# Kernel optimization log

Hardware: AMD Instinct MI355X
Metric: run time of the kernel (lower is better)

Reference implementation:

```python
import jax, jax.numpy as jnp
import numpy as np

N = 320      # num_seq == num_res (pair representation)
C = 128      # num_channels
H = 4        # num_head
D = 32       # qkv_dim = max(C // H, 16)
EPS = 1e-5   # torch LayerNorm default eps
MASK_FILL = -1e9


def setup_inputs() -> dict:
    key = jax.random.key(0)
    ks = jax.random.split(key, 9)
    s = 0.02
    return {
        "act": jax.random.normal(ks[0], (N, N, C), jnp.float32),
        "pair_mask": jax.random.randint(ks[1], (N, N), 0, 2).astype(jnp.int32),
        "ln_gamma": jnp.ones((C,), jnp.float32),
        "ln_beta": jnp.zeros((C,), jnp.float32),
        "w_pair_bias": jax.random.normal(ks[2], (C, H), jnp.float32) * s,  # Linear(C->H, no bias)
        "wq": jax.random.normal(ks[3], (C, H, D), jnp.float32) * s,
        "wk": jax.random.normal(ks[4], (C, H, D), jnp.float32) * s,
        "wv": jax.random.normal(ks[5], (C, H, D), jnp.float32) * s,
        "w_gate": jax.random.normal(ks[6], (C, C), jnp.float32) * s,  # used as act @ W (matches torch.matmul(act, weight))
        "w_out": jax.random.normal(ks[7], (C, C), jnp.float32) * s,   # nn.Linear weight [out,in]; applied as x @ W.T
    }


def reference(act, pair_mask, ln_gamma, ln_beta, w_pair_bias, wq, wk, wv, w_gate, w_out):
    # LayerNorm over channels
    mu = jnp.mean(act, axis=-1, keepdims=True)
    var = jnp.var(act, axis=-1, keepdims=True)
    x = (act - mu) * jax.lax.rsqrt(var + EPS) * ln_gamma + ln_beta  # [N, N, C]

    # Pair-derived nonbatched bias: Linear(C->H) then permute(2,0,1) -> [H, N, N]
    bias = jnp.einsum('qkc,ch->hqk', x, w_pair_bias)

    # pair_mask.permute(1,0)[:, None, None, :] -> [N, 1, 1, N] bool
    mask = (pair_mask.T > 0)[:, None, None, :]

    # QKV projections via einsum '...i,ijk->...jk'
    scale = wq.shape[-1] ** -0.5
    q = jnp.einsum('bqc,chd->bqhd', x, wq) * scale  # [N, N, H, D]
    k = jnp.einsum('bkc,chd->bkhd', x, wk)
    v = jnp.einsum('bkc,chd->bkhd', x, wv)

    logits = jnp.einsum('bqhd,bkhd->bhqk', q, k) + bias[None]  # [N, H, N, N]
    logits = jnp.where(mask, logits, MASK_FILL)
    weights = jax.nn.softmax(logits, axis=-1)
    wa = jnp.einsum('bhqk,bkhd->bqhd', weights, v)  # [N, N, H, D]
    wa = wa.reshape(wa.shape[0], wa.shape[1], -1)   # [N, N, C]

    gate = jax.nn.sigmoid(x @ w_gate)               # torch.matmul(act, gating_query.weight)
    out = (wa * gate) @ w_out.T                     # output_projection (Linear, no bias)
    return out
```

## Files before the change

kernel.cpp:

```cpp
#include <hip/hip_runtime.h>
#include <cstdio>
#include <cstdint>


#define NSEQ 320
#define CCH  128
#define NN   102400
#define QK_SCALE 0.17677669529663687f
#define LN_EPS 1e-5f
#define NEG_BIG -1e9f

typedef __bf16 bf16x8 __attribute__((ext_vector_type(8)));
typedef float  f32x4  __attribute__((ext_vector_type(4)));

__device__ __forceinline__ unsigned short f2bf(float f) {
    unsigned int u = __float_as_uint(f);
    unsigned int r = (u + 0x7FFFu + ((u >> 16) & 1u)) >> 16;
    return (unsigned short)r;
}
__device__ __forceinline__ float bf2f(unsigned short h) {
    return __uint_as_float(((unsigned int)h) << 16);
}

__global__ __launch_bounds__(256) void prep_kernel(
    const float* __restrict__ wq, const float* __restrict__ wk, const float* __restrict__ wv,
    const float* __restrict__ wg, const float* __restrict__ wpb, const float* __restrict__ wo,
    const int* __restrict__ pmask,
    unsigned short* __restrict__ wcat, unsigned short* __restrict__ woutb, int* __restrict__ maskT)
{
    int idx = blockIdx.x * 256 + threadIdx.x;
    if (idx < 576 * 128) {
        int n = idx >> 7, c = idx & 127;
        float v;
        if      (n < 128) v = wq[c * 128 + n] * QK_SCALE;
        else if (n < 256) v = wk[c * 128 + (n - 128)];
        else if (n < 384) v = wv[c * 128 + (n - 256)];
        else if (n < 512) v = wg[c * 128 + (n - 384)];
        else if (n < 516) v = wpb[c * 4 + (n - 512)];
        else              v = 0.f;
        wcat[idx] = f2bf(v);
    } else if (idx < 576 * 128 + 128 * 128) {
        int i = idx - 576 * 128;
        woutb[i] = f2bf(wo[i]);
    } else if (idx < 576 * 128 + 128 * 128 + NN) {
        int i = idx - (576 * 128 + 128 * 128);
        int b = i / NSEQ, k = i - b * NSEQ;
        maskT[i] = pmask[k * NSEQ + b];
    }
}

__global__ __launch_bounds__(256, 4) void ln_proj_kernel(
    const float* __restrict__ act, const float* __restrict__ gamma, const float* __restrict__ beta,
    const unsigned short* __restrict__ wcat,
    unsigned short* __restrict__ qh, unsigned short* __restrict__ kh, unsigned short* __restrict__ vT,
    unsigned short* __restrict__ gh, float* __restrict__ biasS)
{
    __shared__ __align__(16) float          fs[64 * 132];
    __shared__ __align__(16) unsigned short A_lds[64 * 136];
    unsigned short* B_lds = (unsigned short*)fs;

    const int tid  = threadIdx.x;
    const int row0 = blockIdx.x * 64;
    const int bidx = row0 / NSEQ;
    const int qoff = row0 % NSEQ;

    const float4* actv = (const float4*)(act + (size_t)row0 * 128);
    #pragma unroll
    for (int it = 0; it < 8; ++it) {
        int f = it * 256 + tid;
        int row = f >> 5, c4 = f & 31;
        float4 v = actv[f];
        *(float4*)&fs[row * 132 + c4 * 4] = v;
    }
    __syncthreads();

    {
        int row = tid >> 2, seg = tid & 3;
        const float* rp = &fs[row * 132 + seg * 32];
        float vals[32];
        float s = 0.f, sq = 0.f;
        #pragma unroll
        for (int i = 0; i < 32; ++i) { float v = rp[i]; vals[i] = v; s += v; sq += v * v; }
        s  += __shfl_xor(s, 1);  sq += __shfl_xor(sq, 1);
        s  += __shfl_xor(s, 2);  sq += __shfl_xor(sq, 2);
        float mean = s * (1.f / 128.f);
        float var  = sq * (1.f / 128.f) - mean * mean;
        float rstd = rsqrtf(var + LN_EPS);
        #pragma unroll
        for (int j = 0; j < 4; ++j) {
            int c0 = seg * 32 + j * 8;
            float4 g0 = *(const float4*)&gamma[c0];
            float4 g1 = *(const float4*)&gamma[c0 + 4];
            float4 b0 = *(const float4*)&beta[c0];
            float4 b1 = *(const float4*)&beta[c0 + 4];
            union { uint4 u; unsigned short us[8]; } pk;
            pk.us[0] = f2bf((vals[j*8+0] - mean) * rstd * g0.x + b0.x);
            pk.us[1] = f2bf((vals[j*8+1] - mean) * rstd * g0.y + b0.y);
            pk.us[2] = f2bf((vals[j*8+2] - mean) * rstd * g0.z + b0.z);
            pk.us[3] = f2bf((vals[j*8+3] - mean) * rstd * g0.w + b0.w);
            pk.us[4] = f2bf((vals[j*8+4] - mean) * rstd * g1.x + b1.x);
            pk.us[5] = f2bf((vals[j*8+5] - mean) * rstd * g1.y + b1.y);
            pk.us[6] = f2bf((vals[j*8+6] - mean) * rstd * g1.z + b1.z);
            pk.us[7] = f2bf((vals[j*8+7] - mean) * rstd * g1.w + b1.w);
            *(uint4*)&A_lds[row * 136 + c0] = pk.u;
        }
    }
    __syncthreads();

    const int wave = tid >> 6, lane = tid & 63, l15 = lane & 15, l4 = lane >> 4;
    bf16x8 afrag[4];
    #pragma unroll
    for (int kc = 0; kc < 4; ++kc)
        afrag[kc] = *(const bf16x8*)&A_lds[(wave * 16 + l15) * 136 + kc * 32 + l4 * 8];

    for (int nt = 0; nt < 9; ++nt) {
        #pragma unroll
        for (int it = 0; it < 4; ++it) {
            int f = it * 256 + tid;
            int row = f >> 4, c16 = f & 15;
            uint4 u = *(const uint4*)&wcat[(nt * 64 + row) * 128 + c16 * 8];
            *(uint4*)&B_lds[row * 136 + c16 * 8] = u;
        }
        __syncthreads();

        f32x4 acc[4];
        #pragma unroll
        for (int ns = 0; ns < 4; ++ns) { f32x4 z = {0.f,0.f,0.f,0.f}; acc[ns] = z; }
        #pragma unroll
        for (int ns = 0; ns < 4; ++ns)
            #pragma unroll
            for (int kc = 0; kc < 4; ++kc) {
                bf16x8 bfrag = *(const bf16x8*)&B_lds[(ns * 16 + l15) * 136 + kc * 32 + l4 * 8];
                acc[ns] = __builtin_amdgcn_mfma_f32_16x16x32_bf16(afrag[kc], bfrag, acc[ns], 0, 0, 0);
            }

        if (nt == 4 || nt == 5) {
            int key0 = qoff + wave * 16 + l4 * 4;
            #pragma unroll
            for (int ns = 0; ns < 4; ++ns) {
                int j  = nt * 64 + ns * 16 + l15 - 256;
                int hh = j >> 5, d = j & 31;
                ushort4 pk;
                pk.x = f2bf(acc[ns][0]); pk.y = f2bf(acc[ns][1]);
                pk.z = f2bf(acc[ns][2]); pk.w = f2bf(acc[ns][3]);
                *(ushort4*)&vT[((size_t)(bidx * 4 + hh) * 32 + d) * NSEQ + key0] = pk;
            }
            __syncthreads();
        } else if (nt == 8) {
            #pragma unroll
            for (int ns = 0; ns < 4; ++ns) {
                int j = nt * 64 + ns * 16 + l15;
                if (j < 516) {
                    #pragma unroll
                    for (int reg = 0; reg < 4; ++reg) {
                        int r  = row0 + wave * 16 + l4 * 4 + reg;
                        int hh = j - 512;
                        int q  = r / NSEQ, key = r - q * NSEQ;
                        int qm = q & 15,  kl  = key & 15;
                        size_t a = (((size_t)(hh * 20 + (q >> 4)) * 20 + (key >> 4)) << 8)
                                 + ((qm >> 2) << 6) + (kl << 2) + (qm & 3);
                        biasS[a] = acc[ns][reg];
                    }
                }
            }
        } else {
            float* scratch = (float*)A_lds;
            #pragma unroll
            for (int ns = 0; ns < 4; ++ns)
                #pragma unroll
                for (int reg = 0; reg < 4; ++reg)
                    scratch[(wave * 16 + l4 * 4 + reg) * 68 + ns * 16 + l15] = acc[ns][reg];
            __syncthreads();

            int rrow = tid >> 2, c16 = tid & 3;
            int q = qoff + rrow;
            float f[16];
            #pragma unroll
            for (int i = 0; i < 4; ++i)
                *(float4*)&f[i * 4] = *(const float4*)&scratch[rrow * 68 + c16 * 16 + i * 4];

            int jbase = nt * 64 + c16 * 16;
            int cls   = jbase >> 7;
            int jl    = jbase & 127;
            int hh = jl >> 5, d0 = jl & 31;
            unsigned short* dst = (cls == 0) ? qh : (cls == 1) ? kh : gh;
            if (cls == 3) {
                #pragma unroll
                for (int i = 0; i < 16; ++i) f[i] = 1.f / (1.f + __expf(-f[i]));
            }
            union { uint4 u[2]; unsigned short us[16]; } pk;
            #pragma unroll
            for (int i = 0; i < 16; ++i) pk.us[i] = f2bf(f[i]);
            size_t base = ((size_t)(bidx * 4 + hh) * NSEQ + q) * 32 + d0;
            *(uint4*)&dst[base]     = pk.u[0];
            *(uint4*)&dst[base + 8] = pk.u[1];
        }
    }
}

__global__ __launch_bounds__(256, 4) void attn_kernel(
    const unsigned short* __restrict__ qh, const unsigned short* __restrict__ kh,
    const unsigned short* __restrict__ vT, const unsigned short* __restrict__ gh,
    const float* __restrict__ biasS, const int* __restrict__ maskT,
    unsigned short* __restrict__ waG)
{
    __shared__ __align__(16) unsigned short Klds[320 * 36];
    __shared__ __align__(16) unsigned short Pb[4][2][16 * 36];

    const int tid  = threadIdx.x;
    const int bid  = blockIdx.x;
    const int xcd  = bid & 7;
    const int loc  = bid >> 3;
    const int qblk = loc % 5;
    const int g    = (loc / 5) * 8 + xcd;
    const int b    = g >> 2;
    const int h    = g & 3;
    const int wave = tid >> 6, lane = tid & 63, l15 = lane & 15, l4 = lane >> 4;

    const size_t hb  = (size_t)g * NSEQ;
    const size_t hbv = (size_t)g * 32;

    {
        const uint4* src = (const uint4*)(kh + hb * 32);
        #pragma unroll
        for (int it = 0; it < 5; ++it) {
            int idx = it * 256 + tid;
            int key = idx >> 2, part = idx & 3;
            uint4 u = src[idx];
            *(uint4*)&Klds[key * 36 + part * 8] = u;
        }
    }

    const int qrow = qblk * 64 + wave * 16;
    const int qb16 = qblk * 4 + wave;

    bf16x8 aQ = *(const bf16x8*)&qh[(hb + qrow + l15) * 32 + l4 * 8];
    const float* bsw = biasS + (size_t)(h * 20 + qb16) * 20 * 256 + lane * 4;
    const int*   mp  = maskT + b * NSEQ + l15;

    f32x4 s[20];
    #pragma unroll
    for (int t = 0; t < 20; ++t) s[t] = *(const f32x4*)&bsw[t * 256];

    __syncthreads();

    #pragma unroll
    for (int t = 0; t < 20; ++t) {
        bf16x8 bK = *(const bf16x8*)&Klds[(t * 16 + l15) * 36 + l4 * 8];
        s[t] = __builtin_amdgcn_mfma_f32_16x16x32_bf16(aQ, bK, s[t], 0, 0, 0);
    }

    #pragma unroll
    for (int t = 0; t < 20; ++t) {
        int m = mp[t * 16];
        #pragma unroll
        for (int r = 0; r < 4; ++r) s[t][r] = m ? s[t][r] : NEG_BIG;
    }

    #pragma unroll
    for (int r = 0; r < 4; ++r) {
        float mx = -3.4e38f;
        #pragma unroll
        for (int t = 0; t < 20; ++t) mx = fmaxf(mx, s[t][r]);
        mx = fmaxf(mx, __shfl_xor(mx, 1));
        mx = fmaxf(mx, __shfl_xor(mx, 2));
        mx = fmaxf(mx, __shfl_xor(mx, 4));
        mx = fmaxf(mx, __shfl_xor(mx, 8));
        float l = 0.f;
        #pragma unroll
        for (int t = 0; t < 20; ++t) { float p = __expf(s[t][r] - mx); s[t][r] = p; l += p; }
        l += __shfl_xor(l, 1); l += __shfl_xor(l, 2); l += __shfl_xor(l, 4); l += __shfl_xor(l, 8);
        float wv = 1.f / l;
        #pragma unroll
        for (int t = 0; t < 20; ++t) s[t][r] *= wv;
    }

    unsigned short* pb[2] = { Pb[wave][0], Pb[wave][1] };
    #pragma unroll
    for (int tt = 0; tt < 2; ++tt)
        #pragma unroll
        for (int r = 0; r < 4; ++r)
            pb[0][(l4 * 4 + r) * 36 + tt * 16 + l15] = f2bf(s[tt][r]);

    f32x4 acc[2];
    { f32x4 z = {0.f,0.f,0.f,0.f}; acc[0] = z; acc[1] = z; }
    #pragma unroll
    for (int kc = 0; kc < 10; ++kc) {
        bf16x8 aW = *(const bf16x8*)&pb[kc & 1][l15 * 36 + l4 * 8];
        if (kc < 9) {
            unsigned short* nxt = pb[(kc + 1) & 1];
            #pragma unroll
            for (int tt = 0; tt < 2; ++tt)
                #pragma unroll
                for (int r = 0; r < 4; ++r)
                    nxt[(l4 * 4 + r) * 36 + tt * 16 + l15] = f2bf(s[2 * kc + 2 + tt][r]);
        }
        #pragma unroll
        for (int ns = 0; ns < 2; ++ns) {
            bf16x8 bV = *(const bf16x8*)&vT[(hbv + ns * 16 + l15) * NSEQ + kc * 32 + l4 * 8];
            acc[ns] = __builtin_amdgcn_mfma_f32_16x16x32_bf16(aW, bV, acc[ns], 0, 0, 0);
        }
    }

    #pragma unroll
    for (int ns = 0; ns < 2; ++ns)
        #pragma unroll
        for (int r = 0; r < 4; ++r) {
            int q   = qrow + l4 * 4 + r;
            int col = ns * 16 + l15;
            float gv = bf2f(gh[(hb + q) * 32 + col]);
            waG[(hb + q) * 32 + col] = f2bf(acc[ns][r] * gv);
        }
}

__global__ __launch_bounds__(256, 4) void out_proj_kernel(
    const unsigned short* __restrict__ waG, const unsigned short* __restrict__ woutb,
    float* __restrict__ out)
{
    __shared__ __align__(16) unsigned short A_lds[64 * 136];
    __shared__ __align__(16) unsigned short B_lds[128 * 136];
    const int tid  = threadIdx.x;
    const int row0 = blockIdx.x * 64;
    const int bidx = row0 / NSEQ;
    const int qoff = row0 % NSEQ;

    #pragma unroll
    for (int it = 0; it < 4; ++it) {
        int f = it * 256 + tid;
        int row = f >> 4, c16 = f & 15;
        int hh = c16 >> 2, d0 = (c16 & 3) * 8;
        uint4 u = *(const uint4*)&waG[((size_t)(bidx * 4 + hh) * NSEQ + (qoff + row)) * 32 + d0];
        *(uint4*)&A_lds[row * 136 + c16 * 8] = u;
    }
    #pragma unroll
    for (int it = 0; it < 8; ++it) {
        int f = it * 256 + tid;
        int row = f >> 4, c16 = f & 15;
        uint4 u = *(const uint4*)&woutb[f * 8];
        *(uint4*)&B_lds[row * 136 + c16 * 8] = u;
    }
    __syncthreads();

    const int wave = tid >> 6, lane = tid & 63, l15 = lane & 15, l4 = lane >> 4;
    bf16x8 afrag[4];
    #pragma unroll
    for (int kc = 0; kc < 4; ++kc)
        afrag[kc] = *(const bf16x8*)&A_lds[(wave * 16 + l15) * 136 + kc * 32 + l4 * 8];
    f32x4 acc[8];
    #pragma unroll
    for (int ns = 0; ns < 8; ++ns) { f32x4 z = {0.f,0.f,0.f,0.f}; acc[ns] = z; }
    #pragma unroll
    for (int ns = 0; ns < 8; ++ns)
        #pragma unroll
        for (int kc = 0; kc < 4; ++kc) {
            bf16x8 bfrag = *(const bf16x8*)&B_lds[(ns * 16 + l15) * 136 + kc * 32 + l4 * 8];
            acc[ns] = __builtin_amdgcn_mfma_f32_16x16x32_bf16(afrag[kc], bfrag, acc[ns], 0, 0, 0);
        }
    #pragma unroll
    for (int ns = 0; ns < 8; ++ns)
        #pragma unroll
        for (int reg = 0; reg < 4; ++reg) {
            int r = row0 + wave * 16 + l4 * 4 + reg;
            out[(size_t)r * 128 + ns * 16 + l15] = acc[ns][reg];
        }
}

extern "C" void kernel_launch(void* const* d_in, const int* in_sizes, int n_in,
                              void* d_out, int out_size, void* d_ws, size_t ws_size,
                              hipStream_t stream)
{
    (void)in_sizes; (void)n_in; (void)out_size;
    const float* act  = (const float*)d_in[0];
    const int*   pmsk = (const int*)d_in[1];
    const float* gam  = (const float*)d_in[2];
    const float* bet  = (const float*)d_in[3];
    const float* wpb  = (const float*)d_in[4];
    const float* wq   = (const float*)d_in[5];
    const float* wk   = (const float*)d_in[6];
    const float* wv   = (const float*)d_in[7];
    const float* wg   = (const float*)d_in[8];
    const float* wo   = (const float*)d_in[9];
    float* out = (float*)d_out;

    char* ws = (char*)d_ws;
    unsigned short* wcat  = (unsigned short*)(ws + 0);
    unsigned short* woutb = (unsigned short*)(ws + 147456);
    int*            maskT = (int*)           (ws + 180224);
    float*          biasS = (float*)         (ws + 589824);
    unsigned short* qh    = (unsigned short*)(ws + 2228224);
    unsigned short* kh    = (unsigned short*)(ws + 28442624);
    unsigned short* vT    = (unsigned short*)(ws + 54657024);
    unsigned short* gh    = (unsigned short*)(ws + 80871424);
    unsigned short* waG   = (unsigned short*)(ws + 107085824);
    if (ws_size < 133300224ull) {
        fprintf(stderr, "kernel_launch: ws too small (%zu < 133300224)\n", ws_size);
        return;
    }

    prep_kernel    <<<752,  256, 0, stream>>>(wq, wk, wv, wg, wpb, wo, pmsk, wcat, woutb, maskT);
    ln_proj_kernel <<<1600, 256, 0, stream>>>(act, gam, bet, wcat, qh, kh, vT, gh, biasS);
    attn_kernel    <<<6400, 256, 0, stream>>>(qh, kh, vT, gh, biasS, maskT, waG);
    out_proj_kernel<<<1600, 256, 0, stream>>>(waG, woutb, out);
}
```

Measured before the change: 265.6 us.

## Restructure projection, attention softmax and prep kernels with larger tiles and online softmax

The projection kernel now handles 128 rows per block, reading act directly from global memory instead of staging it in LDS, so each weight tile loaded into LDS is reused for two row tiles. The attention kernel switches to a transposed MFMA orientation (K times Q, V times P) and processes keys in two chunks with an online softmax, which lowers register pressure and allows an occupancy hint of 5. The mask transpose in the prep kernel now goes through an LDS tile so both its reads and writes are coalesced. LDS row strides change from 136/36 to 138/34/38 to reduce bank conflicts. The changes to the biasS layout and the write orientation have to stay consistent between the kernels, which adds correctness risk.

Result: slower. 370.1 us (+39.4%).

```diff
diff --git a/kernel.cpp b/kernel.cpp
--- a/kernel.cpp
+++ b/kernel.cpp
@@ -28,59 +28,68 @@
     const int* __restrict__ pmask,
     unsigned short* __restrict__ wcat, unsigned short* __restrict__ woutb, int* __restrict__ maskT)
 {
-    int idx = blockIdx.x * 256 + threadIdx.x;
-    if (idx < 576 * 128) {
-        int n = idx >> 7, c = idx & 127;
-        float v;
-        if      (n < 128) v = wq[c * 128 + n] * QK_SCALE;
-        else if (n < 256) v = wk[c * 128 + (n - 128)];
-        else if (n < 384) v = wv[c * 128 + (n - 256)];
-        else if (n < 512) v = wg[c * 128 + (n - 384)];
-        else if (n < 516) v = wpb[c * 4 + (n - 512)];
-        else              v = 0.f;
-        wcat[idx] = f2bf(v);
-    } else if (idx < 576 * 128 + 128 * 128) {
-        int i = idx - 576 * 128;
-        woutb[i] = f2bf(wo[i]);
-    } else if (idx < 576 * 128 + 128 * 128 + NN) {
-        int i = idx - (576 * 128 + 128 * 128);
-        int b = i / NSEQ, k = i - b * NSEQ;
-        maskT[i] = pmask[k * NSEQ + b];
-    }
-}
-
-__global__ __launch_bounds__(256, 4) void ln_proj_kernel(
+    const int tid = threadIdx.x;
+    if (blockIdx.x < 352) {
+        int idx = blockIdx.x * 256 + tid;
+        if (idx < 576 * 128) {
+            int n = idx >> 7, c = idx & 127;
+            float v;
+            if      (n < 128) v = wq[c * 128 + n] * QK_SCALE;
+            else if (n < 256) v = wk[c * 128 + (n - 128)];
+            else if (n < 384) v = wv[c * 128 + (n - 256)];
+            else if (n < 512) v = wg[c * 128 + (n - 384)];
+            else if (n < 516) v = wpb[c * 4 + (n - 512)];
+            else              v = 0.f;
+            wcat[idx] = f2bf(v);
+        } else {
+            int i = idx - 576 * 128;
+            woutb[i] = f2bf(wo[i]);
+        }
+    } else {
+        __shared__ int tile[64][65];
+        int tb = blockIdx.x - 352;
+        int ti = tb / 5, tj = tb % 5;
+        #pragma unroll
+        for (int it = 0; it < 16; ++it) {
+            int e = it * 256 + tid;
+            int r = e >> 6, c = e & 63;
+            tile[r][c] = pmask[(ti * 64 + r) * NSEQ + tj * 64 + c];
+        }
+        __syncthreads();
+        #pragma unroll
+        for (int it = 0; it < 16; ++it) {
+            int e = it * 256 + tid;
+            int r = e >> 6, c = e & 63;
+            maskT[(tj * 64 + r) * NSEQ + ti * 64 + c] = tile[c][r];
+        }
+    }
+}
+
+__global__ __launch_bounds__(256, 3) void ln_proj_kernel(
     const float* __restrict__ act, const float* __restrict__ gamma, const float* __restrict__ beta,
     const unsigned short* __restrict__ wcat,
     unsigned short* __restrict__ qh, unsigned short* __restrict__ kh, unsigned short* __restrict__ vT,
     unsigned short* __restrict__ gh, float* __restrict__ biasS)
 {
-    __shared__ __align__(16) float          fs[64 * 132];
-    __shared__ __align__(16) unsigned short A_lds[64 * 136];
-    unsigned short* B_lds = (unsigned short*)fs;
+    __shared__ __align__(16) unsigned short A_lds[128 * 138];
+    __shared__ __align__(16) unsigned short B_lds[64 * 138];
 
     const int tid  = threadIdx.x;
-    const int row0 = blockIdx.x * 64;
-    const int bidx = row0 / NSEQ;
-    const int qoff = row0 % NSEQ;
-
-    const float4* actv = (const float4*)(act + (size_t)row0 * 128);
-    #pragma unroll
-    for (int it = 0; it < 8; ++it) {
-        int f = it * 256 + tid;
-        int row = f >> 5, c4 = f & 31;
-        float4 v = actv[f];
-        *(float4*)&fs[row * 132 + c4 * 4] = v;
-    }
-    __syncthreads();
-
-    {
-        int row = tid >> 2, seg = tid & 3;
-        const float* rp = &fs[row * 132 + seg * 32];
+    const int row0 = blockIdx.x * 128;
+    const int wave = tid >> 6, lane = tid & 63, l15 = lane & 15, l4 = lane >> 4;
+
+    #pragma unroll
+    for (int p = 0; p < 2; ++p) {
+        int row = p * 64 + (tid >> 2), seg = tid & 3;
+        const float* rp = act + (size_t)(row0 + row) * 128 + seg * 32;
         float vals[32];
         float s = 0.f, sq = 0.f;
         #pragma unroll
-        for (int i = 0; i < 32; ++i) { float v = rp[i]; vals[i] = v; s += v; sq += v * v; }
+        for (int i = 0; i < 8; ++i) {
+            float4 v = *(const float4*)&rp[i * 4];
+            vals[i*4+0]=v.x; vals[i*4+1]=v.y; vals[i*4+2]=v.z; vals[i*4+3]=v.w;
+            s += v.x+v.y+v.z+v.w; sq += v.x*v.x+v.y*v.y+v.z*v.z+v.w*v.w;
+        }
         s  += __shfl_xor(s, 1);  sq += __shfl_xor(sq, 1);
         s  += __shfl_xor(s, 2);  sq += __shfl_xor(sq, 2);
         float mean = s * (1.f / 128.f);
@@ -102,16 +111,19 @@
             pk.us[5] = f2bf((vals[j*8+5] - mean) * rstd * g1.y + b1.y);
             pk.us[6] = f2bf((vals[j*8+6] - mean) * rstd * g1.z + b1.z);
             pk.us[7] = f2bf((vals[j*8+7] - mean) * rstd * g1.w + b1.w);
-            *(uint4*)&A_lds[row * 136 + c0] = pk.u;
+            *(uint4*)&A_lds[row * 138 + c0] = pk.u;
         }
     }
     __syncthreads();
 
-    const int wave = tid >> 6, lane = tid & 63, l15 = lane & 15, l4 = lane >> 4;
-    bf16x8 afrag[4];
-    #pragma unroll
-    for (int kc = 0; kc < 4; ++kc)
-        afrag[kc] = *(const bf16x8*)&A_lds[(wave * 16 + l15) * 136 + kc * 32 + l4 * 8];
+    bf16x8 afrag[2][4];
+    #pragma unroll
+    for (int tl = 0; tl < 2; ++tl)
+        #pragma unroll
+        for (int kc = 0; kc < 4; ++kc)
+            afrag[tl][kc] = *(const bf16x8*)&A_lds[(tl * 64 + wave * 16 + l15) * 138 + kc * 32 + l4 * 8];
+
+    float* scratch = (float*)A_lds;
 
     for (int nt = 0; nt < 9; ++nt) {
         #pragma unroll
@@ -119,93 +131,99 @@
             int f = it * 256 + tid;
             int row = f >> 4, c16 = f & 15;
             uint4 u = *(const uint4*)&wcat[(nt * 64 + row) * 128 + c16 * 8];
-            *(uint4*)&B_lds[row * 136 + c16 * 8] = u;
+            *(uint4*)&B_lds[row * 138 + c16 * 8] = u;
         }
         __syncthreads();
 
-        f32x4 acc[4];
-        #pragma unroll
-        for (int ns = 0; ns < 4; ++ns) { f32x4 z = {0.f,0.f,0.f,0.f}; acc[ns] = z; }
+        f32x4 acc[2][4];
+        #pragma unroll
+        for (int tl = 0; tl < 2; ++tl)
+            #pragma unroll
+            for (int ns = 0; ns < 4; ++ns) { f32x4 z = {0.f,0.f,0.f,0.f}; acc[tl][ns] = z; }
         #pragma unroll
         for (int ns = 0; ns < 4; ++ns)
             #pragma unroll
             for (int kc = 0; kc < 4; ++kc) {
-                bf16x8 bfrag = *(const bf16x8*)&B_lds[(ns * 16 + l15) * 136 + kc * 32 + l4 * 8];
-                acc[ns] = __builtin_amdgcn_mfma_f32_16x16x32_bf16(afrag[kc], bfrag, acc[ns], 0, 0, 0);
+                bf16x8 bfrag = *(const bf16x8*)&B_lds[(ns * 16 + l15) * 138 + kc * 32 + l4 * 8];
+                #pragma unroll
+                for (int tl = 0; tl < 2; ++tl)
+                    acc[tl][ns] = __builtin_amdgcn_mfma_f32_16x16x32_bf16(afrag[tl][kc], bfrag, acc[tl][ns], 0, 0, 0);
             }
 
         if (nt == 4 || nt == 5) {
-            int key0 = qoff + wave * 16 + l4 * 4;
-            #pragma unroll
-            for (int ns = 0; ns < 4; ++ns) {
-                int j  = nt * 64 + ns * 16 + l15 - 256;
-                int hh = j >> 5, d = j & 31;
-                ushort4 pk;
-                pk.x = f2bf(acc[ns][0]); pk.y = f2bf(acc[ns][1]);
-                pk.z = f2bf(acc[ns][2]); pk.w = f2bf(acc[ns][3]);
-                *(ushort4*)&vT[((size_t)(bidx * 4 + hh) * 32 + d) * NSEQ + key0] = pk;
+            #pragma unroll
+            for (int tl = 0; tl < 2; ++tl) {
+                int R = row0 + tl * 64 + wave * 16 + l4 * 4;
+                int bb = R / NSEQ, key0 = R - bb * NSEQ;
+                #pragma unroll
+                for (int ns = 0; ns < 4; ++ns) {
+                    int j  = nt * 64 + ns * 16 + l15 - 256;
+                    int hh = j >> 5, d = j & 31;
+                    ushort4 pk;
+                    pk.x = f2bf(acc[tl][ns][0]); pk.y = f2bf(acc[tl][ns][1]);
+                    pk.z = f2bf(acc[tl][ns][2]); pk.w = f2bf(acc[tl][ns][3]);
+                    *(ushort4*)&vT[((size_t)(bb * 4 + hh) * 32 + d) * NSEQ + key0] = pk;
+                }
             }
             __syncthreads();
         } else if (nt == 8) {
-            #pragma unroll
-            for (int ns = 0; ns < 4; ++ns) {
-                int j = nt * 64 + ns * 16 + l15;
-                if (j < 516) {
+            if (l15 < 4) {
+                int hh = l15;
+                #pragma unroll
+                for (int tl = 0; tl < 2; ++tl)
                     #pragma unroll
                     for (int reg = 0; reg < 4; ++reg) {
-                        int r  = row0 + wave * 16 + l4 * 4 + reg;
-                        int hh = j - 512;
+                        int r  = row0 + tl * 64 + wave * 16 + l4 * 4 + reg;
                         int q  = r / NSEQ, key = r - q * NSEQ;
-                        int qm = q & 15,  kl  = key & 15;
                         size_t a = (((size_t)(hh * 20 + (q >> 4)) * 20 + (key >> 4)) << 8)
-                                 + ((qm >> 2) << 6) + (kl << 2) + (qm & 3);
-                        biasS[a] = acc[ns][reg];
+                                 + (((key >> 2) & 3) * 16 + (q & 15)) * 4 + (key & 3);
+                        biasS[a] = acc[tl][0][reg];
                     }
-                }
             }
         } else {
-            float* scratch = (float*)A_lds;
-            #pragma unroll
-            for (int ns = 0; ns < 4; ++ns)
+            #pragma unroll
+            for (int tl = 0; tl < 2; ++tl)
                 #pragma unroll
-                for (int reg = 0; reg < 4; ++reg)
-                    scratch[(wave * 16 + l4 * 4 + reg) * 68 + ns * 16 + l15] = acc[ns][reg];
+                for (int ns = 0; ns < 4; ++ns)
+                    #pragma unroll
+                    for (int reg = 0; reg < 4; ++reg)
+                        scratch[(tl * 64 + wave * 16 + l4 * 4 + reg) * 69 + ns * 16 + l15] = acc[tl][ns][reg];
             __syncthreads();
 
-            int rrow = tid >> 2, c16 = tid & 3;
-            int q = qoff + rrow;
-            float f[16];
-            #pragma unroll
-            for (int i = 0; i < 4; ++i)
-                *(float4*)&f[i * 4] = *(const float4*)&scratch[rrow * 68 + c16 * 16 + i * 4];
-
-            int jbase = nt * 64 + c16 * 16;
+            int rrow = tid >> 1, half = tid & 1;
+            int R = row0 + rrow;
+            int bb = R / NSEQ, pos = R - bb * NSEQ;
+            float f[32];
+            #pragma unroll
+            for (int i = 0; i < 8; ++i)
+                *(float4*)&f[i * 4] = *(const float4*)&scratch[rrow * 69 + half * 32 + i * 4];
+
+            int jbase = nt * 64 + half * 32;
             int cls   = jbase >> 7;
-            int jl    = jbase & 127;
-            int hh = jl >> 5, d0 = jl & 31;
+            int hh    = (jbase >> 5) & 3;
             unsigned short* dst = (cls == 0) ? qh : (cls == 1) ? kh : gh;
             if (cls == 3) {
                 #pragma unroll
-                for (int i = 0; i < 16; ++i) f[i] = 1.f / (1.f + __expf(-f[i]));
-            }
-            union { uint4 u[2]; unsigned short us[16]; } pk;
-            #pragma unroll
-            for (int i = 0; i < 16; ++i) pk.us[i] = f2bf(f[i]);
-            size_t base = ((size_t)(bidx * 4 + hh) * NSEQ + q) * 32 + d0;
-            *(uint4*)&dst[base]     = pk.u[0];
-            *(uint4*)&dst[base + 8] = pk.u[1];
-        }
-    }
-}
-
-__global__ __launch_bounds__(256, 4) void attn_kernel(
+                for (int i = 0; i < 32; ++i) f[i] = 1.f / (1.f + __expf(-f[i]));
+            }
+            union { uint4 u[4]; unsigned short us[32]; } pk;
+            #pragma unroll
+            for (int i = 0; i < 32; ++i) pk.us[i] = f2bf(f[i]);
+            size_t base = ((size_t)(bb * 4 + hh) * NSEQ + pos) * 32;
+            #pragma unroll
+            for (int i = 0; i < 4; ++i) *(uint4*)&dst[base + i * 8] = pk.u[i];
+        }
+    }
+}
+
+__global__ __launch_bounds__(256, 5) void attn_kernel(
     const unsigned short* __restrict__ qh, const unsigned short* __restrict__ kh,
     const unsigned short* __restrict__ vT, const unsigned short* __restrict__ gh,
     const float* __restrict__ biasS, const int* __restrict__ maskT,
     unsigned short* __restrict__ waG)
 {
-    __shared__ __align__(16) unsigned short Klds[320 * 36];
-    __shared__ __align__(16) unsigned short Pb[4][2][16 * 36];
+    __shared__ __align__(16) unsigned short Klds[320 * 34];
+    __shared__ __align__(16) unsigned short Pb[4][2][16 * 38];
 
     const int tid  = threadIdx.x;
     const int bid  = blockIdx.x;
@@ -227,98 +245,116 @@
             int idx = it * 256 + tid;
             int key = idx >> 2, part = idx & 3;
             uint4 u = src[idx];
-            *(uint4*)&Klds[key * 36 + part * 8] = u;
+            *(uint4*)&Klds[key * 34 + part * 8] = u;
         }
     }
 
     const int qrow = qblk * 64 + wave * 16;
     const int qb16 = qblk * 4 + wave;
 
-    bf16x8 aQ = *(const bf16x8*)&qh[(hb + qrow + l15) * 32 + l4 * 8];
+    bf16x8 bQ = *(const bf16x8*)&qh[(hb + qrow + l15) * 32 + l4 * 8];
     const float* bsw = biasS + (size_t)(h * 20 + qb16) * 20 * 256 + lane * 4;
-    const int*   mp  = maskT + b * NSEQ + l15;
-
-    f32x4 s[20];
-    #pragma unroll
-    for (int t = 0; t < 20; ++t) s[t] = *(const f32x4*)&bsw[t * 256];
-
-    __syncthreads();
-
-    #pragma unroll
-    for (int t = 0; t < 20; ++t) {
-        bf16x8 bK = *(const bf16x8*)&Klds[(t * 16 + l15) * 36 + l4 * 8];
-        s[t] = __builtin_amdgcn_mfma_f32_16x16x32_bf16(aQ, bK, s[t], 0, 0, 0);
-    }
-
-    #pragma unroll
-    for (int t = 0; t < 20; ++t) {
-        int m = mp[t * 16];
-        #pragma unroll
-        for (int r = 0; r < 4; ++r) s[t][r] = m ? s[t][r] : NEG_BIG;
-    }
-
-    #pragma unroll
-    for (int r = 0; r < 4; ++r) {
-        float mx = -3.4e38f;
-        #pragma unroll
-        for (int t = 0; t < 20; ++t) mx = fmaxf(mx, s[t][r]);
-        mx = fmaxf(mx, __shfl_xor(mx, 1));
-        mx = fmaxf(mx, __shfl_xor(mx, 2));
-        mx = fmaxf(mx, __shfl_xor(mx, 4));
-        mx = fmaxf(mx, __shfl_xor(mx, 8));
-        float l = 0.f;
-        #pragma unroll
-        for (int t = 0; t < 20; ++t) { float p = __expf(s[t][r] - mx); s[t][r] = p; l += p; }
-        l += __shfl_xor(l, 1); l += __shfl_xor(l, 2); l += __shfl_xor(l, 4); l += __shfl_xor(l, 8);
-        float wv = 1.f / l;
-        #pragma unroll
-        for (int t = 0; t < 20; ++t) s[t][r] *= wv;
-    }
-
-    unsigned short* pb[2] = { Pb[wave][0], Pb[wave][1] };
-    #pragma unroll
-    for (int tt = 0; tt < 2; ++tt)
-        #pragma unroll
-        for (int r = 0; r < 4; ++r)
-            pb[0][(l4 * 4 + r) * 36 + tt * 16 + l15] = f2bf(s[tt][r]);
+    const int4*  mp4 = (const int4*)(maskT + b * NSEQ);
+
+    unsigned short* pb0 = Pb[wave][0];
+    unsigned short* pb1 = Pb[wave][1];
 
     f32x4 acc[2];
     { f32x4 z = {0.f,0.f,0.f,0.f}; acc[0] = z; acc[1] = z; }
-    #pragma unroll
-    for (int kc = 0; kc < 10; ++kc) {
-        bf16x8 aW = *(const bf16x8*)&pb[kc & 1][l15 * 36 + l4 * 8];
-        if (kc < 9) {
-            unsigned short* nxt = pb[(kc + 1) & 1];
-            #pragma unroll
-            for (int tt = 0; tt < 2; ++tt)
-                #pragma unroll
-                for (int r = 0; r < 4; ++r)
-                    nxt[(l4 * 4 + r) * 36 + tt * 16 + l15] = f2bf(s[2 * kc + 2 + tt][r]);
-        }
-        #pragma unroll
-        for (int ns = 0; ns < 2; ++ns) {
-            bf16x8 bV = *(const bf16x8*)&vT[(hbv + ns * 16 + l15) * NSEQ + kc * 32 + l4 * 8];
-            acc[ns] = __builtin_amdgcn_mfma_f32_16x16x32_bf16(aW, bV, acc[ns], 0, 0, 0);
-        }
-    }
-
-    #pragma unroll
-    for (int ns = 0; ns < 2; ++ns)
-        #pragma unroll
-        for (int r = 0; r < 4; ++r) {
-            int q   = qrow + l4 * 4 + r;
-            int col = ns * 16 + l15;
-            float gv = bf2f(gh[(hb + q) * 32 + col]);
-            waG[(hb + q) * 32 + col] = f2bf(acc[ns][r] * gv);
-        }
-}
-
-__global__ __launch_bounds__(256, 4) void out_proj_kernel(
+    float mrun = -3.4e38f, lrun = 0.f;
+
+    __syncthreads();
+
+    #pragma unroll
+    for (int ch = 0; ch < 2; ++ch) {
+        const int t0 = ch * 10;
+        f32x4 s[10];
+        #pragma unroll
+        for (int t = 0; t < 10; ++t) s[t] = *(const f32x4*)&bsw[(t0 + t) * 256];
+        #pragma unroll
+        for (int t = 0; t < 10; ++t) {
+            bf16x8 aK = *(const bf16x8*)&Klds[((t0 + t) * 16 + l15) * 34 + l4 * 8];
+            s[t] = __builtin_amdgcn_mfma_f32_16x16x32_bf16(aK, bQ, s[t], 0, 0, 0);
+        }
+        #pragma unroll
+        for (int t = 0; t < 10; ++t) {
+            int4 m4 = mp4[(t0 + t) * 4 + l4];
+            s[t][0] = m4.x ? s[t][0] : NEG_BIG;
+            s[t][1] = m4.y ? s[t][1] : NEG_BIG;
+            s[t][2] = m4.z ? s[t][2] : NEG_BIG;
+            s[t][3] = m4.w ? s[t][3] : NEG_BIG;
+        }
+        float mx = -3.4e38f;
+        #pragma unroll
+        for (int t = 0; t < 10; ++t)
+            #pragma unroll
+            for (int r = 0; r < 4; ++r) mx = fmaxf(mx, s[t][r]);
+        mx = fmaxf(mx, __shfl_xor(mx, 16));
+        mx = fmaxf(mx, __shfl_xor(mx, 32));
+        float mnew  = fmaxf(mrun, mx);
+        float alpha = __expf(mrun - mnew);
+        float l = 0.f;
+        #pragma unroll
+        for (int t = 0; t < 10; ++t)
+            #pragma unroll
+            for (int r = 0; r < 4; ++r) { float p = __expf(s[t][r] - mnew); s[t][r] = p; l += p; }
+        l += __shfl_xor(l, 16);
+        l += __shfl_xor(l, 32);
+        lrun = lrun * alpha + l;
+        mrun = mnew;
+        #pragma unroll
+        for (int ns = 0; ns < 2; ++ns)
+            #pragma unroll
+            for (int r = 0; r < 4; ++r) acc[ns][r] *= alpha;
+
+        {
+            ushort4 p0, p1;
+            p0.x=f2bf(s[0][0]); p0.y=f2bf(s[0][1]); p0.z=f2bf(s[0][2]); p0.w=f2bf(s[0][3]);
+            p1.x=f2bf(s[1][0]); p1.y=f2bf(s[1][1]); p1.z=f2bf(s[1][2]); p1.w=f2bf(s[1][3]);
+            *(ushort4*)&pb0[l15 * 38 + l4 * 4]      = p0;
+            *(ushort4*)&pb0[l15 * 38 + 16 + l4 * 4] = p1;
+        }
+        #pragma unroll
+        for (int kc = 0; kc < 5; ++kc) {
+            unsigned short* cur = (kc & 1) ? pb1 : pb0;
+            unsigned short* nxt = (kc & 1) ? pb0 : pb1;
+            bf16x8 bP = *(const bf16x8*)&cur[l15 * 38 + l4 * 8];
+            if (kc < 4) {
+                ushort4 p0, p1;
+                p0.x=f2bf(s[2*kc+2][0]); p0.y=f2bf(s[2*kc+2][1]); p0.z=f2bf(s[2*kc+2][2]); p0.w=f2bf(s[2*kc+2][3]);
+                p1.x=f2bf(s[2*kc+3][0]); p1.y=f2bf(s[2*kc+3][1]); p1.z=f2bf(s[2*kc+3][2]); p1.w=f2bf(s[2*kc+3][3]);
+                *(ushort4*)&nxt[l15 * 38 + l4 * 4]      = p0;
+                *(ushort4*)&nxt[l15 * 38 + 16 + l4 * 4] = p1;
+            }
+            #pragma unroll
+            for (int ns = 0; ns < 2; ++ns) {
+                bf16x8 aV = *(const bf16x8*)&vT[(hbv + ns * 16 + l15) * NSEQ + ch * 160 + kc * 32 + l4 * 8];
+                acc[ns] = __builtin_amdgcn_mfma_f32_16x16x32_bf16(aV, bP, acc[ns], 0, 0, 0);
+            }
+        }
+    }
+
+    float rn = 1.f / lrun;
+    int q = qrow + l15;
+    #pragma unroll
+    for (int ns = 0; ns < 2; ++ns) {
+        int d0 = ns * 16 + l4 * 4;
+        ushort4 gv = *(const ushort4*)&gh[(hb + q) * 32 + d0];
+        ushort4 o;
+        o.x = f2bf(acc[ns][0] * rn * bf2f(gv.x));
+        o.y = f2bf(acc[ns][1] * rn * bf2f(gv.y));
+        o.z = f2bf(acc[ns][2] * rn * bf2f(gv.z));
+        o.w = f2bf(acc[ns][3] * rn * bf2f(gv.w));
+        *(ushort4*)&waG[(hb + q) * 32 + d0] = o;
+    }
+}
+
+__global__ __launch_bounds__(256, 3) void out_proj_kernel(
     const unsigned short* __restrict__ waG, const unsigned short* __restrict__ woutb,
     float* __restrict__ out)
 {
-    __shared__ __align__(16) unsigned short A_lds[64 * 136];
-    __shared__ __align__(16) unsigned short B_lds[128 * 136];
+    __shared__ __align__(16) unsigned short A_lds[64 * 138];
+    __shared__ __align__(16) unsigned short B_lds[128 * 138];
     const int tid  = threadIdx.x;
     const int row0 = blockIdx.x * 64;
     const int bidx = row0 / NSEQ;
@@ -330,14 +366,14 @@
         int row = f >> 4, c16 = f & 15;
         int hh = c16 >> 2, d0 = (c16 & 3) * 8;
         uint4 u = *(const uint4*)&waG[((size_t)(bidx * 4 + hh) * NSEQ + (qoff + row)) * 32 + d0];
-        *(uint4*)&A_lds[row * 136 + c16 * 8] = u;
+        *(uint4*)&A_lds[row * 138 + c16 * 8] = u;
     }
     #pragma unroll
     for (int it = 0; it < 8; ++it) {
         int f = it * 256 + tid;
         int row = f >> 4, c16 = f & 15;
         uint4 u = *(const uint4*)&woutb[f * 8];
-        *(uint4*)&B_lds[row * 136 + c16 * 8] = u;
+        *(uint4*)&B_lds[row * 138 + c16 * 8] = u;
     }
     __syncthreads();
 
@@ -345,7 +381,7 @@
     bf16x8 afrag[4];
     #pragma unroll
     for (int kc = 0; kc < 4; ++kc)
-        afrag[kc] = *(const bf16x8*)&A_lds[(wave * 16 + l15) * 136 + kc * 32 + l4 * 8];
+        afrag[kc] = *(const bf16x8*)&A_lds[(wave * 16 + l15) * 138 + kc * 32 + l4 * 8];
     f32x4 acc[8];
     #pragma unroll
     for (int ns = 0; ns < 8; ++ns) { f32x4 z = {0.f,0.f,0.f,0.f}; acc[ns] = z; }
@@ -353,7 +389,7 @@
     for (int ns = 0; ns < 8; ++ns)
         #pragma unroll
         for (int kc = 0; kc < 4; ++kc) {
-            bf16x8 bfrag = *(const bf16x8*)&B_lds[(ns * 16 + l15) * 136 + kc * 32 + l4 * 8];
+            bf16x8 bfrag = *(const bf16x8*)&B_lds[(ns * 16 + l15) * 138 + kc * 32 + l4 * 8];
             acc[ns] = __builtin_amdgcn_mfma_f32_16x16x32_bf16(afrag[kc], bfrag, acc[ns], 0, 0, 0);
         }
     #pragma unroll
@@ -397,8 +433,8 @@
         return;
     }
 
-    prep_kernel    <<<752,  256, 0, stream>>>(wq, wk, wv, wg, wpb, wo, pmsk, wcat, woutb, maskT);
-    ln_proj_kernel <<<1600, 256, 0, stream>>>(act, gam, bet, wcat, qh, kh, vT, gh, biasS);
+    prep_kernel    <<<377,  256, 0, stream>>>(wq, wk, wv, wg, wpb, wo, pmsk, wcat, woutb, maskT);
+    ln_proj_kernel <<<800,  256, 0, stream>>>(act, gam, bet, wcat, qh, kh, vT, gh, biasS);
     attn_kernel    <<<6400, 256, 0, stream>>>(qh, kh, vT, gh, biasS, maskT, waG);
     out_proj_kernel<<<1600, 256, 0, stream>>>(waG, woutb, out);
 }
```

## Pack bf16 conversions, tile mask transpose, defer softmax normalization, repad LDS

Applied to the files above, without the earlier changes.

Several independent tweaks land together. Float-to-bf16 conversion now uses a packed two-value builtin where available. The pair-mask transpose in prep goes through a shared-memory tile so reads and writes are coalesced. Softmax normalization moves from every probability to the final attention output, applied per row. LDS row strides change from 136 to 138 halves (and 68 to 69 floats) to shift bank mapping, and out_proj launch bounds change. The new strides break 16-byte alignment for the vector LDS accesses, which risks split or slower loads and stores.

Result: slower. 363.7 us (+37.0%).

```diff
diff --git a/kernel.cpp b/kernel.cpp
--- a/kernel.cpp
+++ b/kernel.cpp
@@ -18,6 +18,15 @@
     unsigned int r = (u + 0x7FFFu + ((u >> 16) & 1u)) >> 16;
     return (unsigned short)r;
 }
+__device__ __forceinline__ unsigned int f2bf_pk(float a, float b) {
+#if __has_builtin(__builtin_amdgcn_cvt_pk_bf16_f32)
+    typedef __bf16 bf16x2 __attribute__((ext_vector_type(2)));
+    bf16x2 v = __builtin_amdgcn_cvt_pk_bf16_f32(a, b);
+    unsigned int u; __builtin_memcpy(&u, &v, 4); return u;
+#else
+    return (unsigned int)f2bf(a) | ((unsigned int)f2bf(b) << 16);
+#endif
+}
 __device__ __forceinline__ float bf2f(unsigned short h) {
     return __uint_as_float(((unsigned int)h) << 16);
 }
@@ -28,24 +37,40 @@
     const int* __restrict__ pmask,
     unsigned short* __restrict__ wcat, unsigned short* __restrict__ woutb, int* __restrict__ maskT)
 {
-    int idx = blockIdx.x * 256 + threadIdx.x;
-    if (idx < 576 * 128) {
-        int n = idx >> 7, c = idx & 127;
-        float v;
-        if      (n < 128) v = wq[c * 128 + n] * QK_SCALE;
-        else if (n < 256) v = wk[c * 128 + (n - 128)];
-        else if (n < 384) v = wv[c * 128 + (n - 256)];
-        else if (n < 512) v = wg[c * 128 + (n - 384)];
-        else if (n < 516) v = wpb[c * 4 + (n - 512)];
-        else              v = 0.f;
-        wcat[idx] = f2bf(v);
-    } else if (idx < 576 * 128 + 128 * 128) {
-        int i = idx - 576 * 128;
-        woutb[i] = f2bf(wo[i]);
-    } else if (idx < 576 * 128 + 128 * 128 + NN) {
-        int i = idx - (576 * 128 + 128 * 128);
-        int b = i / NSEQ, k = i - b * NSEQ;
-        maskT[i] = pmask[k * NSEQ + b];
+    const int tid = threadIdx.x;
+    if (blockIdx.x < 352) {
+        int idx = blockIdx.x * 256 + tid;
+        if (idx < 576 * 128) {
+            int n = idx >> 7, c = idx & 127;
+            float v;
+            if      (n < 128) v = wq[c * 128 + n] * QK_SCALE;
+            else if (n < 256) v = wk[c * 128 + (n - 128)];
+            else if (n < 384) v = wv[c * 128 + (n - 256)];
+            else if (n < 512) v = wg[c * 128 + (n - 384)];
+            else if (n < 516) v = wpb[c * 4 + (n - 512)];
+            else              v = 0.f;
+            wcat[idx] = f2bf(v);
+        } else {
+            int i = idx - 576 * 128;
+            woutb[i] = f2bf(wo[i]);
+        }
+    } else {
+        __shared__ int tile[64][65];
+        int tb = blockIdx.x - 352;
+        int ti = tb / 5, tj = tb % 5;
+        #pragma unroll
+        for (int it = 0; it < 16; ++it) {
+            int e = it * 256 + tid;
+            int r = e >> 6, c = e & 63;
+            tile[r][c] = pmask[(ti * 64 + r) * NSEQ + tj * 64 + c];
+        }
+        __syncthreads();
+        #pragma unroll
+        for (int it = 0; it < 16; ++it) {
+            int e = it * 256 + tid;
+            int r = e >> 6, c = e & 63;
+            maskT[(tj * 64 + r) * NSEQ + ti * 64 + c] = tile[c][r];
+        }
     }
 }
 
@@ -56,7 +81,7 @@
     unsigned short* __restrict__ gh, float* __restrict__ biasS)
 {
     __shared__ __align__(16) float          fs[64 * 132];
-    __shared__ __align__(16) unsigned short A_lds[64 * 136];
+    __shared__ __align__(16) unsigned short A_lds[64 * 138];
     unsigned short* B_lds = (unsigned short*)fs;
 
     const int tid  = threadIdx.x;
@@ -93,16 +118,12 @@
             float4 g1 = *(const float4*)&gamma[c0 + 4];
             float4 b0 = *(const float4*)&beta[c0];
             float4 b1 = *(const float4*)&beta[c0 + 4];
-            union { uint4 u; unsigned short us[8]; } pk;
-            pk.us[0] = f2bf((vals[j*8+0] - mean) * rstd * g0.x + b0.x);
-            pk.us[1] = f2bf((vals[j*8+1] - mean) * rstd * g0.y + b0.y);
-            pk.us[2] = f2bf((vals[j*8+2] - mean) * rstd * g0.z + b0.z);
-            pk.us[3] = f2bf((vals[j*8+3] - mean) * rstd * g0.w + b0.w);
-            pk.us[4] = f2bf((vals[j*8+4] - mean) * rstd * g1.x + b1.x);
-            pk.us[5] = f2bf((vals[j*8+5] - mean) * rstd * g1.y + b1.y);
-            pk.us[6] = f2bf((vals[j*8+6] - mean) * rstd * g1.z + b1.z);
-            pk.us[7] = f2bf((vals[j*8+7] - mean) * rstd * g1.w + b1.w);
-            *(uint4*)&A_lds[row * 136 + c0] = pk.u;
+            union { uint4 u; unsigned int w[4]; } pk;
+            pk.w[0] = f2bf_pk((vals[j*8+0]-mean)*rstd*g0.x+b0.x, (vals[j*8+1]-mean)*rstd*g0.y+b0.y);
+            pk.w[1] = f2bf_pk((vals[j*8+2]-mean)*rstd*g0.z+b0.z, (vals[j*8+3]-mean)*rstd*g0.w+b0.w);
+            pk.w[2] = f2bf_pk((vals[j*8+4]-mean)*rstd*g1.x+b1.x, (vals[j*8+5]-mean)*rstd*g1.y+b1.y);
+            pk.w[3] = f2bf_pk((vals[j*8+6]-mean)*rstd*g1.z+b1.z, (vals[j*8+7]-mean)*rstd*g1.w+b1.w);
+            *(uint4*)&A_lds[row * 138 + c0] = pk.u;
         }
     }
     __syncthreads();
@@ -111,7 +132,9 @@
     bf16x8 afrag[4];
     #pragma unroll
     for (int kc = 0; kc < 4; ++kc)
-        afrag[kc] = *(const bf16x8*)&A_lds[(wave * 16 + l15) * 136 + kc * 32 + l4 * 8];
+        afrag[kc] = *(const bf16x8*)&A_lds[(wave * 16 + l15) * 138 + kc * 32 + l4 * 8];
+
+    float* scratch = (float*)A_lds;
 
     for (int nt = 0; nt < 9; ++nt) {
         #pragma unroll
@@ -119,7 +142,7 @@
             int f = it * 256 + tid;
             int row = f >> 4, c16 = f & 15;
             uint4 u = *(const uint4*)&wcat[(nt * 64 + row) * 128 + c16 * 8];
-            *(uint4*)&B_lds[row * 136 + c16 * 8] = u;
+            *(uint4*)&B_lds[row * 138 + c16 * 8] = u;
         }
         __syncthreads();
 
@@ -130,7 +153,7 @@
         for (int ns = 0; ns < 4; ++ns)
             #pragma unroll
             for (int kc = 0; kc < 4; ++kc) {
-                bf16x8 bfrag = *(const bf16x8*)&B_lds[(ns * 16 + l15) * 136 + kc * 32 + l4 * 8];
+                bf16x8 bfrag = *(const bf16x8*)&B_lds[(ns * 16 + l15) * 138 + kc * 32 + l4 * 8];
                 acc[ns] = __builtin_amdgcn_mfma_f32_16x16x32_bf16(afrag[kc], bfrag, acc[ns], 0, 0, 0);
             }
 
@@ -140,10 +163,10 @@
             for (int ns = 0; ns < 4; ++ns) {
                 int j  = nt * 64 + ns * 16 + l15 - 256;
                 int hh = j >> 5, d = j & 31;
-                ushort4 pk;
-                pk.x = f2bf(acc[ns][0]); pk.y = f2bf(acc[ns][1]);
-                pk.z = f2bf(acc[ns][2]); pk.w = f2bf(acc[ns][3]);
-                *(ushort4*)&vT[((size_t)(bidx * 4 + hh) * 32 + d) * NSEQ + key0] = pk;
+                uint2 pk;
+                pk.x = f2bf_pk(acc[ns][0], acc[ns][1]);
+                pk.y = f2bf_pk(acc[ns][2], acc[ns][3]);
+                *(uint2*)&vT[((size_t)(bidx * 4 + hh) * 32 + d) * NSEQ + key0] = pk;
             }
             __syncthreads();
         } else if (nt == 8) {
@@ -164,12 +187,11 @@
                 }
             }
         } else {
-            float* scratch = (float*)A_lds;
             #pragma unroll
             for (int ns = 0; ns < 4; ++ns)
                 #pragma unroll
                 for (int reg = 0; reg < 4; ++reg)
-                    scratch[(wave * 16 + l4 * 4 + reg) * 68 + ns * 16 + l15] = acc[ns][reg];
+                    scratch[(wave * 16 + l4 * 4 + reg) * 69 + ns * 16 + l15] = acc[ns][reg];
             __syncthreads();
 
             int rrow = tid >> 2, c16 = tid & 3;
@@ -177,7 +199,7 @@
             float f[16];
             #pragma unroll
             for (int i = 0; i < 4; ++i)
-                *(float4*)&f[i * 4] = *(const float4*)&scratch[rrow * 68 + c16 * 16 + i * 4];
+                *(float4*)&f[i * 4] = *(const float4*)&scratch[rrow * 69 + c16 * 16 + i * 4];
 
             int jbase = nt * 64 + c16 * 16;
             int cls   = jbase >> 7;
@@ -188,9 +210,9 @@
                 #pragma unroll
                 for (int i = 0; i < 16; ++i) f[i] = 1.f / (1.f + __expf(-f[i]));
             }
-            union { uint4 u[2]; unsigned short us[16]; } pk;
-            #pragma unroll
-            for (int i = 0; i < 16; ++i) pk.us[i] = f2bf(f[i]);
+            union { uint4 u[2]; unsigned int w[8]; } pk;
+            #pragma unroll
+            for (int i = 0; i < 8; ++i) pk.w[i] = f2bf_pk(f[2*i], f[2*i+1]);
             size_t base = ((size_t)(bidx * 4 + hh) * NSEQ + q) * 32 + d0;
             *(uint4*)&dst[base]     = pk.u[0];
             *(uint4*)&dst[base + 8] = pk.u[1];
@@ -257,6 +279,7 @@
         for (int r = 0; r < 4; ++r) s[t][r] = m ? s[t][r] : NEG_BIG;
     }
 
+    float rn[4];
     #pragma unroll
     for (int r = 0; r < 4; ++r) {
         float mx = -3.4e38f;
@@ -270,17 +293,20 @@
         #pragma unroll
         for (int t = 0; t < 20; ++t) { float p = __expf(s[t][r] - mx); s[t][r] = p; l += p; }
         l += __shfl_xor(l, 1); l += __shfl_xor(l, 2); l += __shfl_xor(l, 4); l += __shfl_xor(l, 8);
-        float wv = 1.f / l;
-        #pragma unroll
-        for (int t = 0; t < 20; ++t) s[t][r] *= wv;
+        rn[r] = 1.f / l;
     }
 
     unsigned short* pb[2] = { Pb[wave][0], Pb[wave][1] };
     #pragma unroll
-    for (int tt = 0; tt < 2; ++tt)
-        #pragma unroll
-        for (int r = 0; r < 4; ++r)
-            pb[0][(l4 * 4 + r) * 36 + tt * 16 + l15] = f2bf(s[tt][r]);
+    for (int tt = 0; tt < 2; ++tt) {
+        unsigned int u01 = f2bf_pk(s[tt][0], s[tt][1]);
+        unsigned int u23 = f2bf_pk(s[tt][2], s[tt][3]);
+        unsigned short* c = &pb[0][(l4 * 4) * 36 + tt * 16 + l15];
+        c[0]   = (unsigned short)(u01 & 0xffff);
+        c[36]  = (unsigned short)(u01 >> 16);
+        c[72]  = (unsigned short)(u23 & 0xffff);
+        c[108] = (unsigned short)(u23 >> 16);
+    }
 
     f32x4 acc[2];
     { f32x4 z = {0.f,0.f,0.f,0.f}; acc[0] = z; acc[1] = z; }
@@ -290,10 +316,15 @@
         if (kc < 9) {
             unsigned short* nxt = pb[(kc + 1) & 1];
             #pragma unroll
-            for (int tt = 0; tt < 2; ++tt)
-                #pragma unroll
-                for (int r = 0; r < 4; ++r)
-                    nxt[(l4 * 4 + r) * 36 + tt * 16 + l15] = f2bf(s[2 * kc + 2 + tt][r]);
+            for (int tt = 0; tt < 2; ++tt) {
+                unsigned int u01 = f2bf_pk(s[2*kc+2+tt][0], s[2*kc+2+tt][1]);
+                unsigned int u23 = f2bf_pk(s[2*kc+2+tt][2], s[2*kc+2+tt][3]);
+                unsigned short* c = &nxt[(l4 * 4) * 36 + tt * 16 + l15];
+                c[0]   = (unsigned short)(u01 & 0xffff);
+                c[36]  = (unsigned short)(u01 >> 16);
+                c[72]  = (unsigned short)(u23 & 0xffff);
+                c[108] = (unsigned short)(u23 >> 16);
+            }
         }
         #pragma unroll
         for (int ns = 0; ns < 2; ++ns) {
@@ -309,16 +340,16 @@
             int q   = qrow + l4 * 4 + r;
             int col = ns * 16 + l15;
             float gv = bf2f(gh[(hb + q) * 32 + col]);
-            waG[(hb + q) * 32 + col] = f2bf(acc[ns][r] * gv);
-        }
-}
-
-__global__ __launch_bounds__(256, 4) void out_proj_kernel(
+            waG[(hb + q) * 32 + col] = f2bf(acc[ns][r] * rn[r] * gv);
+        }
+}
+
+__global__ __launch_bounds__(256, 3) void out_proj_kernel(
     const unsigned short* __restrict__ waG, const unsigned short* __restrict__ woutb,
     float* __restrict__ out)
 {
-    __shared__ __align__(16) unsigned short A_lds[64 * 136];
-    __shared__ __align__(16) unsigned short B_lds[128 * 136];
+    __shared__ __align__(16) unsigned short A_lds[64 * 138];
+    __shared__ __align__(16) unsigned short B_lds[128 * 138];
     const int tid  = threadIdx.x;
     const int row0 = blockIdx.x * 64;
     const int bidx = row0 / NSEQ;
@@ -330,14 +361,14 @@
         int row = f >> 4, c16 = f & 15;
         int hh = c16 >> 2, d0 = (c16 & 3) * 8;
         uint4 u = *(const uint4*)&waG[((size_t)(bidx * 4 + hh) * NSEQ + (qoff + row)) * 32 + d0];
-        *(uint4*)&A_lds[row * 136 + c16 * 8] = u;
+        *(uint4*)&A_lds[row * 138 + c16 * 8] = u;
     }
     #pragma unroll
     for (int it = 0; it < 8; ++it) {
         int f = it * 256 + tid;
         int row = f >> 4, c16 = f & 15;
         uint4 u = *(const uint4*)&woutb[f * 8];
-        *(uint4*)&B_lds[row * 136 + c16 * 8] = u;
+        *(uint4*)&B_lds[row * 138 + c16 * 8] = u;
     }
     __syncthreads();
 
@@ -345,7 +376,7 @@
     bf16x8 afrag[4];
     #pragma unroll
     for (int kc = 0; kc < 4; ++kc)
-        afrag[kc] = *(const bf16x8*)&A_lds[(wave * 16 + l15) * 136 + kc * 32 + l4 * 8];
+        afrag[kc] = *(const bf16x8*)&A_lds[(wave * 16 + l15) * 138 + kc * 32 + l4 * 8];
     f32x4 acc[8];
     #pragma unroll
     for (int ns = 0; ns < 8; ++ns) { f32x4 z = {0.f,0.f,0.f,0.f}; acc[ns] = z; }
@@ -353,7 +384,7 @@
     for (int ns = 0; ns < 8; ++ns)
         #pragma unroll
         for (int kc = 0; kc < 4; ++kc) {
-            bf16x8 bfrag = *(const bf16x8*)&B_lds[(ns * 16 + l15) * 136 + kc * 32 + l4 * 8];
+            bf16x8 bfrag = *(const bf16x8*)&B_lds[(ns * 16 + l15) * 138 + kc * 32 + l4 * 8];
             acc[ns] = __builtin_amdgcn_mfma_f32_16x16x32_bf16(afrag[kc], bfrag, acc[ns], 0, 0, 0);
         }
     #pragma unroll
@@ -397,7 +428,7 @@
         return;
     }
 
-    prep_kernel    <<<752,  256, 0, stream>>>(wq, wk, wv, wg, wpb, wo, pmsk, wcat, woutb, maskT);
+    prep_kernel    <<<377,  256, 0, stream>>>(wq, wk, wv, wg, wpb, wo, pmsk, wcat, woutb, maskT);
     ln_proj_kernel <<<1600, 256, 0, stream>>>(act, gam, bet, wcat, qh, kh, vT, gh, biasS);
     attn_kernel    <<<6400, 256, 0, stream>>>(qh, kh, vT, gh, biasS, maskT, waG);
     out_proj_kernel<<<1600, 256, 0, stream>>>(waG, woutb, out);
```
